# Kernel tuning notes

Hardware: AMD Instinct MI355X
Metric: run time of the kernel (lower is better)

## Reference

```python
import jax, jax.numpy as jnp
import numpy as np

K = 3        # kernel_size
DIL = 1      # dilation
PAD = 1      # padding (replicate)
RANKS = 3
STAGES = 9
C_OUT = 32


def setup_inputs() -> dict:
    key = jax.random.key(0)
    k1, k2, k3 = jax.random.split(key, 3)
    b, cin, H, W = 2, 3, 160, 160
    x = jax.random.normal(k1, (b, cin, H, W), dtype=jnp.float32)
    head_w = jax.random.normal(k2, (C_OUT, cin), dtype=jnp.float32) * (1.0 / np.sqrt(cin))
    tail_w = jax.random.normal(k3, (cin, C_OUT), dtype=jnp.float32) * (1.0 / np.sqrt(C_OUT))
    alphas = jnp.full((STAGES,), 0.01, dtype=jnp.float32)
    betas = jnp.full((STAGES,), 0.01, dtype=jnp.float32)
    return {"x": x, "head_w": head_w, "tail_w": tail_w, "alphas": alphas, "betas": betas}


def _unfold_like_torch(xp, H, W):
    # xp: [b, C, H+2p, W+2p] replicate-padded. Reproduce torch nn.Unfold output
    # layout [b, C*k*k, H*W] (channel-major, then ki, kj; L row-major over h,w).
    b, C = xp.shape[0], xp.shape[1]
    cols = [xp[:, :, i * DIL:i * DIL + H, j * DIL:j * DIL + W]
            for i in range(K) for j in range(K)]
    patches = jnp.stack(cols, axis=2)            # [b, C, k*k, H, W]
    return patches.reshape(b, C * K * K, H * W)  # torch unfold layout


def reference(x, head_w, tail_w, alphas, betas):
    b, cin, H, W = x.shape
    # head 1x1 conv (no bias) + relu
    xh = jax.nn.relu(jnp.einsum('bchw,oc->bohw', x, head_w))
    xp = jnp.pad(xh, ((0, 0), (0, 0), (PAD, PAD), (PAD, PAD)), mode='edge')
    Xu = _unfold_like_torch(xp, H, W)                 # [b, C*kk, H*W]
    # Faithful to torch: X = unfold.view(b, C, H, W, -1) (row-major reinterpret)
    X = Xu.reshape(b, C_OUT, H, W, K * K)
    U = jnp.repeat(X.mean(axis=-1, keepdims=True), RANKS, axis=-1)  # [b,C,H,W,r]
    V = jnp.repeat(X.mean(axis=1, keepdims=True), RANKS, axis=1)    # [b,r,H,W,kk]
    for i in range(STAGES):
        num_V = jnp.einsum('bchwr,bchwk->brhwk', U, X)
        UV = jnp.einsum('bchwr,brhwk->bchwk', U, V)
        den_V = jnp.einsum('bchwr,bchwk->brhwk', U, UV)
        V = V - betas[i] * (den_V - num_V)
        num_U = jnp.einsum('bchwk,brhwk->bchwr', X, V)
        UV = jnp.einsum('bchwr,brhwk->bchwk', U, V)
        den_U = jnp.einsum('bchwk,brhwk->bchwr', UV, V)
        U = U - alphas[i] * (den_U - num_U)
    center = (K // 2) * K + K // 2
    UVc = jnp.einsum('bchwr,brhwk->bchwk', U, V)[..., center]  # [b,C,H,W]
    out = jax.nn.relu(jnp.einsum('bchw,oc->bohw', UVc, tail_w))
    return out
```

## Files before the change

### kernel.cpp

```cpp
#include <hip/hip_runtime.h>
#include <hip/hip_bf16.h>

#define NB    2
#define HW    25600
#define WDIM  160
#define NSTG  9

template <int CTRL>
__device__ __forceinline__ float dpp_add(float v) {
    int moved = __builtin_amdgcn_update_dpp(0, __float_as_int(v), CTRL, 0xf, 0xf, true);
    return v + __int_as_float(moved);
}

__device__ __forceinline__ float reduce8(float v) {
    v = dpp_add<0xB1>(v);
    v = dpp_add<0x4E>(v);
    v = dpp_add<0x141>(v);
    return v;
}

__global__ __launch_bounds__(256) void fused_kernel(const float* __restrict__ x,
                                                    const float* __restrict__ head_w,
                                                    const float* __restrict__ tail_w,
                                                    const float* __restrict__ alphas,
                                                    const float* __restrict__ betas,
                                                    float* __restrict__ out) {
    int tid = blockIdx.x * 256 + threadIdx.x;
    int sub = threadIdx.x & 7;
    int pid = tid >> 3;
    int b   = blockIdx.x / 800;
    int s2  = pid - b * HW;

    int c0 = sub * 4;
    float hw[4][3];
#pragma unroll
    for (int j = 0; j < 4; ++j)
#pragma unroll
        for (int ci = 0; ci < 3; ++ci)
            hw[j][ci] = head_w[(c0 + j) * 3 + ci];

    const float* xb = x + b * 3 * HW;

    float X[9][4];
    int g9  = s2 * 9;
    int kk0 = g9 / HW;
    int r0  = g9 - kk0 * HW;
    int h0  = r0 / WDIM;
    int w0  = r0 - h0 * WDIM;
#pragma unroll
    for (int k2 = 0; k2 < 9; ++k2) {
        int r    = r0 + k2;
        int wrap = (r >= HW);
        int wn   = w0 + k2;
        int cw   = (wn >= WDIM);
        int w_nw = wn - (cw ? WDIM : 0);
        int h_nw = h0 + cw;
        int h    = wrap ? 0 : h_nw;
        int w    = wrap ? (r - HW) : w_nw;
        int kk   = kk0 + wrap;
        int ki   = kk / 3;
        int kj   = kk - ki * 3;
        int hh   = min(max(h + ki - 1, 0), 159);
        int ww   = min(max(w + kj - 1, 0), 159);
        int p    = hh * WDIM + ww;
        float x0 = xb[p], x1 = xb[HW + p], x2 = xb[2 * HW + p];
#pragma unroll
        for (int j = 0; j < 4; ++j)
            X[k2][j] = fmaxf(hw[j][0] * x0 + hw[j][1] * x1 + hw[j][2] * x2, 0.f);
    }

    float u[4];
#pragma unroll
    for (int j = 0; j < 4; ++j) {
        float a = X[0][j];
#pragma unroll
        for (int k = 1; k < 9; ++k) a += X[k][j];
        u[j] = a * (1.f / 9.f);
    }
    float v[9];
#pragma unroll
    for (int k = 0; k < 9; ++k) {
        float pr = (X[k][0] + X[k][1]) + (X[k][2] + X[k][3]);
        v[k] = reduce8(pr) * (1.f / 32.f);
    }

#pragma unroll
    for (int i = 0; i < NSTG; ++i) {
        float beta  = betas[i];
        float alpha = alphas[i];
        float sp = (u[0] * u[0] + u[1] * u[1]) + (u[2] * u[2] + u[3] * u[3]);
        float s  = reduce8(sp);
        float vs = 1.f - 3.f * beta * s;
#pragma unroll
        for (int k = 0; k < 9; ++k) {
            float qp = (u[0] * X[k][0] + u[1] * X[k][1]) + (u[2] * X[k][2] + u[3] * X[k][3]);
            float q  = reduce8(qp);
            v[k] = v[k] * vs + beta * q;
        }
        float t = 0.f;
#pragma unroll
        for (int k = 0; k < 9; ++k) t += v[k] * v[k];
        float us = 1.f - 3.f * alpha * t;
#pragma unroll
        for (int j = 0; j < 4; ++j) {
            float m = 0.f;
#pragma unroll
            for (int k = 0; k < 9; ++k) m += X[k][j] * v[k];
            u[j] = u[j] * us + alpha * m;
        }
    }

    float v4 = v[4];
    float uvc[4];
#pragma unroll
    for (int j = 0; j < 4; ++j) uvc[j] = 3.f * u[j] * v4;
    float o[3];
#pragma unroll
    for (int oo = 0; oo < 3; ++oo) {
        const float* tw = tail_w + oo * 32 + c0;
        float pr = (uvc[0] * tw[0] + uvc[1] * tw[1]) + (uvc[2] * tw[2] + uvc[3] * tw[3]);
        o[oo] = fmaxf(reduce8(pr), 0.f);
    }
    if (sub == 0) {
        float* op = out + b * 3 * HW + s2;
        op[0]      = o[0];
        op[HW]     = o[1];
        op[2 * HW] = o[2];
    }
}

extern "C" void kernel_launch(void* const* d_in, const int* in_sizes, int n_in,
                              void* d_out, int out_size, void* d_ws, size_t ws_size,
                              hipStream_t stream) {
    const float* x      = (const float*)d_in[0];
    const float* head_w = (const float*)d_in[1];
    const float* tail_w = (const float*)d_in[2];
    const float* alphas = (const float*)d_in[3];
    const float* betas  = (const float*)d_in[4];
    float*       out    = (float*)d_out;

    fused_kernel<<<dim3(NB * HW * 8 / 256), dim3(256), 0, stream>>>(
        x, head_w, tail_w, alphas, betas, out);
}
```

Measured before the change: 78.96 us.

## Assign 8 channels per thread with 4-lane groups to cut cross-lane reductions

Each pixel is now handled by 4 lanes with 8 channels each instead of 8 lanes with 4 channels, so every cross-lane reduction needs one fewer DPP step and each lane does more FMAs per shuffle. The grid is halved, launch bounds request 3 blocks per SIMD, and the unfold index math is simplified by precomputing the kernel offsets. The trade-off is that the X tile doubles to 72 floats per thread, which raises register pressure and can lower occupancy or cause spills, while the total thread count drops.

Measured after the change: 75.84 us. 4.0% less time.

```diff
diff --git a/kernel.cpp b/kernel.cpp
--- a/kernel.cpp
+++ b/kernel.cpp
@@ -12,66 +12,71 @@
     return v + __int_as_float(moved);
 }
 
-__device__ __forceinline__ float reduce8(float v) {
+__device__ __forceinline__ float reduce4(float v) {
     v = dpp_add<0xB1>(v);
     v = dpp_add<0x4E>(v);
-    v = dpp_add<0x141>(v);
     return v;
 }
 
-__global__ __launch_bounds__(256) void fused_kernel(const float* __restrict__ x,
-                                                    const float* __restrict__ head_w,
-                                                    const float* __restrict__ tail_w,
-                                                    const float* __restrict__ alphas,
-                                                    const float* __restrict__ betas,
-                                                    float* __restrict__ out) {
-    int tid = blockIdx.x * 256 + threadIdx.x;
-    int sub = threadIdx.x & 7;
-    int pid = tid >> 3;
-    int b   = blockIdx.x / 800;
+__global__ __launch_bounds__(256, 3) void fused_kernel(const float* __restrict__ x,
+                                                       const float* __restrict__ head_w,
+                                                       const float* __restrict__ tail_w,
+                                                       const float* __restrict__ alphas,
+                                                       const float* __restrict__ betas,
+                                                       float* __restrict__ out) {
+    int sub = threadIdx.x & 3;
+    int pid = blockIdx.x * 64 + (threadIdx.x >> 2);
+    int b   = blockIdx.x / 400;
     int s2  = pid - b * HW;
 
-    int c0 = sub * 4;
-    float hw[4][3];
+    int c0 = sub * 8;
+    float hw[8][3];
 #pragma unroll
-    for (int j = 0; j < 4; ++j)
+    for (int j = 0; j < 8; ++j)
 #pragma unroll
         for (int ci = 0; ci < 3; ++ci)
             hw[j][ci] = head_w[(c0 + j) * 3 + ci];
 
-    const float* xb = x + b * 3 * HW;
+    const float* xb0 = x + b * 3 * HW;
+    const float* xb1 = xb0 + HW;
+    const float* xb2 = xb1 + HW;
 
-    float X[9][4];
     int g9  = s2 * 9;
     int kk0 = g9 / HW;
     int r0  = g9 - kk0 * HW;
     int h0  = r0 / WDIM;
     int w0  = r0 - h0 * WDIM;
+    int ki0 = kk0 / 3;
+    int dh0 = ki0 - 1,            dw0 = kk0 - ki0 * 3 - 1;
+    int kk1 = kk0 + 1;
+    int ki1 = kk1 / 3;
+    int dh1 = ki1 - 1,            dw1 = kk1 - ki1 * 3 - 1;
+
+    float X[9][8];
 #pragma unroll
     for (int k2 = 0; k2 < 9; ++k2) {
-        int r    = r0 + k2;
-        int wrap = (r >= HW);
-        int wn   = w0 + k2;
-        int cw   = (wn >= WDIM);
-        int w_nw = wn - (cw ? WDIM : 0);
-        int h_nw = h0 + cw;
-        int h    = wrap ? 0 : h_nw;
-        int w    = wrap ? (r - HW) : w_nw;
-        int kk   = kk0 + wrap;
-        int ki   = kk / 3;
-        int kj   = kk - ki * 3;
-        int hh   = min(max(h + ki - 1, 0), 159);
-        int ww   = min(max(w + kj - 1, 0), 159);
-        int p    = hh * WDIM + ww;
-        float x0 = xb[p], x1 = xb[HW + p], x2 = xb[2 * HW + p];
+        int r  = r0 + k2;
+        int wn = w0 + k2;
+        int cw = (wn >= WDIM);
+        int w1 = cw ? wn - WDIM : wn;
+        int h1 = h0 + cw;
+        bool wr = (r >= HW);
+        int h  = wr ? 0 : h1;
+        int w  = wr ? r - HW : w1;
+        int dh = wr ? dh1 : dh0;
+        int dw = wr ? dw1 : dw0;
+        int hh = min(max(h + dh, 0), 159);
+        int ww = min(max(w + dw, 0), 159);
+        int p  = hh * WDIM + ww;
+        float x0 = xb0[p], x1 = xb1[p], x2 = xb2[p];
 #pragma unroll
-        for (int j = 0; j < 4; ++j)
+        for (int j = 0; j < 8; ++j)
             X[k2][j] = fmaxf(hw[j][0] * x0 + hw[j][1] * x1 + hw[j][2] * x2, 0.f);
     }
 
-    float u[4];
+    float u[8];
 #pragma unroll
-    for (int j = 0; j < 4; ++j) {
+    for (int j = 0; j < 8; ++j) {
         float a = X[0][j];
 #pragma unroll
         for (int k = 1; k < 9; ++k) a += X[k][j];
@@ -80,46 +85,53 @@
     float v[9];
 #pragma unroll
     for (int k = 0; k < 9; ++k) {
-        float pr = (X[k][0] + X[k][1]) + (X[k][2] + X[k][3]);
-        v[k] = reduce8(pr) * (1.f / 32.f);
+        float pr = ((X[k][0] + X[k][1]) + (X[k][2] + X[k][3]))
+                 + ((X[k][4] + X[k][5]) + (X[k][6] + X[k][7]));
+        v[k] = reduce4(pr) * (1.f / 32.f);
     }
 
 #pragma unroll
     for (int i = 0; i < NSTG; ++i) {
+        float b3 = 3.f * betas[i];
+        float a3 = 3.f * alphas[i];
         float beta  = betas[i];
         float alpha = alphas[i];
-        float sp = (u[0] * u[0] + u[1] * u[1]) + (u[2] * u[2] + u[3] * u[3]);
-        float s  = reduce8(sp);
-        float vs = 1.f - 3.f * beta * s;
+        float sp = ((u[0] * u[0] + u[1] * u[1]) + (u[2] * u[2] + u[3] * u[3]))
+                 + ((u[4] * u[4] + u[5] * u[5]) + (u[6] * u[6] + u[7] * u[7]));
+        float s  = reduce4(sp);
+        float vs = 1.f - b3 * s;
 #pragma unroll
         for (int k = 0; k < 9; ++k) {
-            float qp = (u[0] * X[k][0] + u[1] * X[k][1]) + (u[2] * X[k][2] + u[3] * X[k][3]);
-            float q  = reduce8(qp);
+            float qp = u[0] * X[k][0];
+#pragma unroll
+            for (int j = 1; j < 8; ++j) qp += u[j] * X[k][j];
+            float q = reduce4(qp);
             v[k] = v[k] * vs + beta * q;
         }
-        float t = 0.f;
+        float t = (((v[0] * v[0] + v[1] * v[1]) + (v[2] * v[2] + v[3] * v[3]))
+                +  ((v[4] * v[4] + v[5] * v[5]) + (v[6] * v[6] + v[7] * v[7])))
+                +  v[8] * v[8];
+        float us = 1.f - a3 * t;
 #pragma unroll
-        for (int k = 0; k < 9; ++k) t += v[k] * v[k];
-        float us = 1.f - 3.f * alpha * t;
+        for (int j = 0; j < 8; ++j) {
+            float m = X[0][j] * v[0];
 #pragma unroll
-        for (int j = 0; j < 4; ++j) {
-            float m = 0.f;
-#pragma unroll
-            for (int k = 0; k < 9; ++k) m += X[k][j] * v[k];
+            for (int k = 1; k < 9; ++k) m += X[k][j] * v[k];
             u[j] = u[j] * us + alpha * m;
         }
     }
 
     float v4 = v[4];
-    float uvc[4];
+    float uvc[8];
 #pragma unroll
-    for (int j = 0; j < 4; ++j) uvc[j] = 3.f * u[j] * v4;
+    for (int j = 0; j < 8; ++j) uvc[j] = 3.f * u[j] * v4;
     float o[3];
 #pragma unroll
     for (int oo = 0; oo < 3; ++oo) {
         const float* tw = tail_w + oo * 32 + c0;
-        float pr = (uvc[0] * tw[0] + uvc[1] * tw[1]) + (uvc[2] * tw[2] + uvc[3] * tw[3]);
-        o[oo] = fmaxf(reduce8(pr), 0.f);
+        float pr = ((uvc[0] * tw[0] + uvc[1] * tw[1]) + (uvc[2] * tw[2] + uvc[3] * tw[3]))
+                 + ((uvc[4] * tw[4] + uvc[5] * tw[5]) + (uvc[6] * tw[6] + uvc[7] * tw[7]));
+        o[oo] = fmaxf(reduce4(pr), 0.f);
     }
     if (sub == 0) {
         float* op = out + b * 3 * HW + s2;
@@ -139,6 +151,6 @@
     const float* betas  = (const float*)d_in[4];
     float*       out    = (float*)d_out;
 
-    fused_kernel<<<dim3(NB * HW * 8 / 256), dim3(256), 0, stream>>>(
+    fused_kernel<<<dim3(NB * HW * 4 / 256), dim3(256), 0, stream>>>(
         x, head_w, tail_w, alphas, betas, out);
 }
```
